# Kernel optimization log

Measured on AMD Instinct MI355X. Metric: run time of the kernel, lower is better.

The kernel has to match this reference:

```python
import jax, jax.numpy as jnp
import numpy as np

EPS = 1e-3
POWER = 2


def setup_inputs() -> dict:
    key = jax.random.key(0)
    k1, k2, k3 = jax.random.split(key, 3)
    inputs = jax.random.normal(k1, (8192, 512), dtype=jnp.float32)
    keys = jax.random.normal(k2, (4096, 512), dtype=jnp.float32)
    values = jax.random.normal(k3, (4096, 1000), dtype=jnp.float32)
    return {"inputs": inputs, "keys": keys, "values": values}


def reference(inputs, keys, values):
    # x: [B, D]; keys: [P, D]; values: [P, C]
    x = inputs.reshape(inputs.shape[0], -1)
    k = keys.reshape(keys.shape[0], -1)
    sq = (
        jnp.sum(x * x, axis=1, keepdims=True)
        + jnp.sum(k * k, axis=1)[None, :]
        - 2.0 * (x @ k.T)
    )
    d = jnp.sqrt(jnp.maximum(sq, 0.0))  # torch.cdist (p=2)
    dist = EPS + d ** POWER
    attn = 1.0 / dist
    attn = attn / jnp.sum(attn, axis=1, keepdims=True)
    logits = attn @ values  # [B, C]
    return logits
```

## Files before the change

kernel.cpp:

```cpp
#include <hip/hip_runtime.h>
#include <stdint.h>

#define EPS_F 1e-3f

#define NB 8192
#define NP 4096
#define ND 512
#define NC 1000
#define NCP 1024

#define SXK 21.8966f
#define INV_SXK2 (1.0f / (SXK * SXK))
#define SA 72571.43f
#define INV_SA (1.0f / SA)

typedef __attribute__((ext_vector_type(4))) int intx4;

static __device__ __forceinline__ void gl_lds16(const void* g, void* l) {
  __builtin_amdgcn_global_load_lds(
      (const __attribute__((address_space(1))) void*)g,
      (__attribute__((address_space(3))) void*)l,
      16, 0, 0);
}

static __device__ __forceinline__ signed char q8(float x, float s, float lo) {
  float v = fminf(fmaxf(x * s, lo), 127.0f);
  return (signed char)__float2int_rn(v);
}

__global__ __launch_bounds__(256) void prep_kernel(
    const float* __restrict__ X, const float* __restrict__ Kk,
    const float* __restrict__ V,
    signed char* __restrict__ Xq, signed char* __restrict__ Kq,
    float* __restrict__ xnorm, float* __restrict__ knorm,
    float* __restrict__ rowsum, unsigned* __restrict__ vmax) {
  const int b = blockIdx.x;
  const int tid = threadIdx.x;
  __shared__ float tile[32][33];

  if (b < 3072) {
    const float* src;
    signed char* dst;
    float* nrm;
    int rbase;
    if (b < 2048) {
      src = X; dst = Xq; nrm = xnorm; rbase = b * 4;
      if (tid < 4) rowsum[b * 4 + tid] = 0.0f;
    } else {
      src = Kk; dst = Kq; nrm = knorm; rbase = (b - 2048) * 4;
    }
    const int w = tid >> 6, l = tid & 63;
    const int r = rbase + w;
    const float* p = src + (size_t)r * ND + l * 8;
    float4 v0 = *(const float4*)p;
    float4 v1 = *(const float4*)(p + 4);
    float s = v0.x * v0.x + v0.y * v0.y + v0.z * v0.z + v0.w * v0.w +
              v1.x * v1.x + v1.y * v1.y + v1.z * v1.z + v1.w * v1.w;
    union { signed char c[8]; uint2 u; } pk;
    pk.c[0] = q8(v0.x, SXK, -127.f); pk.c[1] = q8(v0.y, SXK, -127.f);
    pk.c[2] = q8(v0.z, SXK, -127.f); pk.c[3] = q8(v0.w, SXK, -127.f);
    pk.c[4] = q8(v1.x, SXK, -127.f); pk.c[5] = q8(v1.y, SXK, -127.f);
    pk.c[6] = q8(v1.z, SXK, -127.f); pk.c[7] = q8(v1.w, SXK, -127.f);
    *(uint2*)(dst + (size_t)r * ND + l * 8) = pk.u;
    for (int off = 32; off > 0; off >>= 1) s += __shfl_xor(s, off, 64);
    if (l == 0) nrm[r] = s;
  } else {
    const int t = b - 3072;
    const int pt = t & 127, ct = t >> 7;
    const int p0 = pt * 32, c0 = ct * 32;
    const int i = tid >> 3, j4 = (tid & 7) * 4;
    const float* vp = V + (size_t)(p0 + i) * NC;
    for (int u = 0; u < 4; ++u) {
      int c = c0 + j4 + u;
      tile[i][j4 + u] = (c < NC) ? vp[c] : 0.0f;
    }
    __syncthreads();
    if (tid < 32) {
      float m = 0.0f;
      for (int r = 0; r < 32; ++r) m = fmaxf(m, fabsf(tile[r][tid]));
      atomicMax(&vmax[c0 + tid], __float_as_uint(m));
    }
  }
}

__global__ __launch_bounds__(256) void vt_quant_kernel(
    const float* __restrict__ V, const unsigned* __restrict__ vmax,
    signed char* __restrict__ Vtq) {
  const int t = blockIdx.x;
  const int tid = threadIdx.x;
  __shared__ float tile[32][33];
  const int pt = t & 127, ct = t >> 7;
  const int p0 = pt * 32, c0 = ct * 32;
  const int i = tid >> 3, j4 = (tid & 7) * 4;
  const float* vp = V + (size_t)(p0 + i) * NC;
  for (int u = 0; u < 4; ++u) {
    int c = c0 + j4 + u;
    tile[i][j4 + u] = (c < NC) ? vp[c] : 0.0f;
  }
  __syncthreads();
  const int j = tid >> 3, i4 = (tid & 7) * 4;
  const float vm = __uint_as_float(vmax[c0 + j]);
  const float s = (vm > 0.0f) ? 127.0f / vm : 0.0f;
  union { signed char c[4]; unsigned u; } pk;
  for (int u = 0; u < 4; ++u) pk.c[u] = q8(tile[i4 + u][j], s, -127.f);
  *(unsigned*)(Vtq + (size_t)(c0 + j) * NP + p0 + i4) = pk.u;
}

template <int KD>
static __device__ __forceinline__ void gemm_core_i8(
    const signed char* __restrict__ gA, const signed char* __restrict__ gB,
    signed char* lA, signed char* lB, intx4 (&acc)[4][4]) {
  const int tid = threadIdx.x;
  const int w = tid >> 6, lane = tid & 63;
  const int wm = w >> 1, wn = w & 1;
  const int lm = lane & 15, q = lane >> 4;
  const int srow = lane >> 2;
  const int c_lds = lane & 3;
  const int sw = (lm >> 1) & 3;

  for (int k0 = 0; k0 < KD; k0 += 64) {
    for (int t = 0; t < 2; ++t) {
      const int row0 = w * 32 + t * 16;
      const int row = row0 + srow;
      const int cg = c_lds ^ ((row >> 1) & 3);
      gl_lds16(gA + (size_t)row * KD + k0 + cg * 16, &lA[row0 * 64]);
      gl_lds16(gB + (size_t)row * KD + k0 + cg * 16, &lB[row0 * 64]);
    }
    __syncthreads();
    intx4 af[4], bf[4];
    for (int t = 0; t < 4; ++t) {
      const int ra = wm * 64 + t * 16 + lm;
      af[t] = *(const intx4*)&lA[ra * 64 + (q ^ sw) * 16];
      const int rb = wn * 64 + t * 16 + lm;
      bf[t] = *(const intx4*)&lB[rb * 64 + (q ^ sw) * 16];
    }
    for (int i = 0; i < 4; ++i)
      for (int j = 0; j < 4; ++j)
        acc[i][j] = __builtin_amdgcn_mfma_i32_16x16x64_i8(af[i], bf[j],
                                                          acc[i][j], 0, 0, 0);
    __syncthreads();
  }
}

__global__ __launch_bounds__(256, 4) void gemm1_kernel(
    const signed char* __restrict__ A, const signed char* __restrict__ B,
    const float* __restrict__ xnorm, const float* __restrict__ knorm,
    signed char* __restrict__ attnq, float* __restrict__ rowsum) {
  __shared__ __align__(16) signed char lA[128 * 64];
  __shared__ __align__(16) signed char lB[128 * 64];
  const int tid = threadIdx.x;
  const int w = tid >> 6, lane = tid & 63;
  const int wm = w >> 1, wn = w & 1;
  const int lm = lane & 15, q = lane >> 4;
  const int bm = blockIdx.y * 128, bn = blockIdx.x * 128;

  intx4 acc[4][4];
  for (int i = 0; i < 4; ++i)
    for (int j = 0; j < 4; ++j) acc[i][j] = (intx4)(0);

  gemm_core_i8<ND>(A + (size_t)bm * ND, B + (size_t)bn * ND, lA, lB, acc);

  for (int i = 0; i < 4; ++i) {
    for (int r = 0; r < 4; ++r) {
      const int grow = bm + wm * 64 + i * 16 + q * 4 + r;
      const float xn = xnorm[grow];
      float rs = 0.0f;
      for (int j = 0; j < 4; ++j) {
        const int gcol = bn + wn * 64 + j * 16 + lm;
        const float dot = (float)acc[i][j][r] * INV_SXK2;
        float sq = fmaxf(xn + knorm[gcol] - 2.0f * dot, 0.0f);
        float a = 1.0f / (EPS_F + sq);
        rs += a;
        attnq[(size_t)grow * NP + gcol] =
            (signed char)__float2int_rn(fminf(a * SA, 127.0f));
      }
      rs += __shfl_xor(rs, 1, 16);
      rs += __shfl_xor(rs, 2, 16);
      rs += __shfl_xor(rs, 4, 16);
      rs += __shfl_xor(rs, 8, 16);
      if (lm == 0) atomicAdd(&rowsum[grow], rs);
    }
  }
}

__global__ __launch_bounds__(256, 4) void gemm2_kernel(
    const signed char* __restrict__ A, const signed char* __restrict__ B,
    const float* __restrict__ rowsum, const unsigned* __restrict__ vmax,
    float* __restrict__ out) {
  __shared__ __align__(16) signed char lA[128 * 64];
  __shared__ __align__(16) signed char lB[128 * 64];
  const int tid = threadIdx.x;
  const int w = tid >> 6, lane = tid & 63;
  const int wm = w >> 1, wn = w & 1;
  const int lm = lane & 15, q = lane >> 4;
  const int id = blockIdx.x;
  const int bn = (id >> 6) * 128;
  const int bm = (id & 63) * 128;

  intx4 acc[4][4];
  for (int i = 0; i < 4; ++i)
    for (int j = 0; j < 4; ++j) acc[i][j] = (intx4)(0);

  gemm_core_i8<NP>(A + (size_t)bm * NP, B + (size_t)bn * NP, lA, lB, acc);

  float coef[4];
  for (int j = 0; j < 4; ++j) {
    const int gcol = bn + wn * 64 + j * 16 + lm;
    coef[j] = __uint_as_float(vmax[gcol]) * (INV_SA * (1.0f / 127.0f));
  }

  for (int i = 0; i < 4; ++i) {
    for (int r = 0; r < 4; ++r) {
      const int grow = bm + wm * 64 + i * 16 + q * 4 + r;
      const float inv = 1.0f / rowsum[grow];
      for (int j = 0; j < 4; ++j) {
        const int gcol = bn + wn * 64 + j * 16 + lm;
        if (gcol < NC)
          out[(size_t)grow * NC + gcol] = (float)acc[i][j][r] * coef[j] * inv;
      }
    }
  }
}

extern "C" void kernel_launch(void* const* d_in, const int* in_sizes, int n_in,
                              void* d_out, int out_size, void* d_ws,
                              size_t ws_size, hipStream_t stream) {
  const float* X = (const float*)d_in[0];
  const float* Kk = (const float*)d_in[1];
  const float* V = (const float*)d_in[2];
  float* out = (float*)d_out;
  char* ws = (char*)d_ws;

  signed char* Xq = (signed char*)(ws + 0);
  signed char* Kq = (signed char*)(ws + 4194304);
  signed char* Vtq = (signed char*)(ws + 6291456);
  signed char* attnq = (signed char*)(ws + 10485760);
  float* xnorm = (float*)(ws + 44040192);
  float* knorm = (float*)(ws + 44072960);
  float* rowsum = (float*)(ws + 44089344);
  unsigned* vmax = (unsigned*)(ws + 44122112);

  hipMemsetAsync(vmax, 0, NCP * sizeof(unsigned), stream);
  prep_kernel<<<7168, 256, 0, stream>>>(X, Kk, V, Xq, Kq, xnorm, knorm,
                                        rowsum, vmax);
  vt_quant_kernel<<<4096, 256, 0, stream>>>(V, vmax, Vtq);
  gemm1_kernel<<<dim3(NP / 128, NB / 128), 256, 0, stream>>>(Xq, Kq, xnorm,
                                                             knorm, attnq,
                                                             rowsum);
  gemm2_kernel<<<512, 256, 0, stream>>>(attnq, Vtq, rowsum, vmax, out);
}
```

Before: 192.8 us.

## Permute attention K-order so the gemm1 epilogue stores packed dwords

The gemm1 epilogue now packs each lane's four quantized attention bytes into one 32-bit store instead of four scattered byte stores. This places them at a permuted column position within each 64-wide block. The V transpose/quantization kernel is retiled to 64x16 so it writes the quantized V with the same permutation along P, which keeps the reduction in gemm2 consistent. The epilogue also hoists the knorm loads, folds the distance math into one FMA with the eps clamp, and uses hardware approximate reciprocals in both epilogues. The approximate reciprocal adds a small loss of accuracy.

```diff
diff --git a/kernel.cpp b/kernel.cpp
--- a/kernel.cpp
+++ b/kernel.cpp
@@ -11,6 +11,7 @@
 
 #define SXK 21.8966f
 #define INV_SXK2 (1.0f / (SXK * SXK))
+#define C2DOT (2.0f * INV_SXK2)
 #define SA 72571.43f
 #define INV_SA (1.0f / SA)
 
@@ -27,6 +28,7 @@
   float v = fminf(fmaxf(x * s, lo), 127.0f);
   return (signed char)__float2int_rn(v);
 }
+
 
 __global__ __launch_bounds__(256) void prep_kernel(
     const float* __restrict__ X, const float* __restrict__ Kk,
@@ -88,22 +90,26 @@
     signed char* __restrict__ Vtq) {
   const int t = blockIdx.x;
   const int tid = threadIdx.x;
-  __shared__ float tile[32][33];
-  const int pt = t & 127, ct = t >> 7;
-  const int p0 = pt * 32, c0 = ct * 32;
-  const int i = tid >> 3, j4 = (tid & 7) * 4;
-  const float* vp = V + (size_t)(p0 + i) * NC;
+  __shared__ float tile[64][17];
+  const int pt = t & 63, ct = t >> 6;
+  const int p0 = pt * 64, c0 = ct * 16;
+  const int pl = tid >> 2, cf = (tid & 3) * 4;
+  const float* vp = V + (size_t)(p0 + pl) * NC;
   for (int u = 0; u < 4; ++u) {
-    int c = c0 + j4 + u;
-    tile[i][j4 + u] = (c < NC) ? vp[c] : 0.0f;
+    int c = c0 + cf + u;
+    tile[pl][cf + u] = (c < NC) ? vp[c] : 0.0f;
   }
   __syncthreads();
-  const int j = tid >> 3, i4 = (tid & 7) * 4;
-  const float vm = __uint_as_float(vmax[c0 + j]);
+  const int cl = tid & 15, l = tid >> 4;
+  const int c = c0 + cl;
+  const float vm = __uint_as_float(vmax[c]);
   const float s = (vm > 0.0f) ? 127.0f / vm : 0.0f;
-  union { signed char c[4]; unsigned u; } pk;
-  for (int u = 0; u < 4; ++u) pk.c[u] = q8(tile[i4 + u][j], s, -127.f);
-  *(unsigned*)(Vtq + (size_t)(c0 + j) * NP + p0 + i4) = pk.u;
+  unsigned pk = 0;
+  for (int u = 0; u < 4; ++u) {
+    signed char b = q8(tile[16 * u + l][cl], s, -127.f);
+    pk |= ((unsigned)(unsigned char)b) << (8 * u);
+  }
+  *(unsigned*)(Vtq + (size_t)c * NP + p0 + 4 * l) = pk;
 }
 
 template <int KD>
@@ -160,20 +166,24 @@
 
   gemm_core_i8<ND>(A + (size_t)bm * ND, B + (size_t)bn * ND, lA, lB, acc);
 
+  float kn[4];
+  for (int j = 0; j < 4; ++j) kn[j] = knorm[bn + wn * 64 + j * 16 + lm];
+
   for (int i = 0; i < 4; ++i) {
     for (int r = 0; r < 4; ++r) {
       const int grow = bm + wm * 64 + i * 16 + q * 4 + r;
-      const float xn = xnorm[grow];
+      const float xne = xnorm[grow] + EPS_F;
       float rs = 0.0f;
+      unsigned pk = 0;
       for (int j = 0; j < 4; ++j) {
-        const int gcol = bn + wn * 64 + j * 16 + lm;
-        const float dot = (float)acc[i][j][r] * INV_SXK2;
-        float sq = fmaxf(xn + knorm[gcol] - 2.0f * dot, 0.0f);
-        float a = 1.0f / (EPS_F + sq);
+        float t = fmaf((float)acc[i][j][r], -C2DOT, xne + kn[j]);
+        t = fmaxf(t, EPS_F);
+        float a = __builtin_amdgcn_rcpf(t);
         rs += a;
-        attnq[(size_t)grow * NP + gcol] =
-            (signed char)__float2int_rn(fminf(a * SA, 127.0f));
+        unsigned bq = (unsigned)__float2int_rn(fminf(a * SA, 127.0f));
+        pk |= bq << (8 * j);
       }
+      *(unsigned*)(attnq + (size_t)grow * NP + bn + wn * 64 + 4 * lm) = pk;
       rs += __shfl_xor(rs, 1, 16);
       rs += __shfl_xor(rs, 2, 16);
       rs += __shfl_xor(rs, 4, 16);
@@ -212,7 +222,7 @@
   for (int i = 0; i < 4; ++i) {
     for (int r = 0; r < 4; ++r) {
       const int grow = bm + wm * 64 + i * 16 + q * 4 + r;
-      const float inv = 1.0f / rowsum[grow];
+      const float inv = __builtin_amdgcn_rcpf(rowsum[grow]);
       for (int j = 0; j < 4; ++j) {
         const int gcol = bn + wn * 64 + j * 16 + lm;
         if (gcol < NC)
```

After: 195.1 us. Within noise of the previous version (+1.2%).
